# Kernel tuning notes

Hardware: AMD Instinct MI355X
Metric: run time of the kernel (lower is better)

The kernel has to match this reference:

```python
import jax, jax.numpy as jnp
import numpy as np

B, H, NQ, NL, NA = 262144, 256, 4, 2, 16


def _apply_1q(s, U, q):
    # s: [B, 2,2,2,2]; U: [B,2,2] (batched) or [2,2] (shared)
    s = jnp.moveaxis(s, 1 + q, -1)
    if U.ndim == 3:
        s = jnp.einsum('bij,b...j->b...i', U, s)
    else:
        s = jnp.einsum('ij,b...j->b...i', U, s)
    return jnp.moveaxis(s, -1, 1 + q)


def _apply_cnot(s, c, t):
    s = jnp.moveaxis(s, (1 + c, 1 + t), (-2, -1))
    s = jnp.stack([s[..., 0, :], s[..., 1, ::-1]], axis=-2)  # flip target when control=1
    return jnp.moveaxis(s, (-2, -1), (1 + c, 1 + t))


def _rx(theta):
    # batched RX: theta [B] -> [B,2,2]
    c = jnp.cos(theta / 2).astype(jnp.complex64)
    s = (-1j) * jnp.sin(theta / 2)
    return jnp.stack([jnp.stack([c, s], -1), jnp.stack([s, c], -1)], -2)


def _rot(phi, theta, omega):
    # PennyLane Rot = RZ(omega) @ RY(theta) @ RZ(phi), scalar angles -> [2,2]
    c, s = jnp.cos(theta / 2), jnp.sin(theta / 2)
    return jnp.array(1, jnp.complex64) * jnp.stack([
        jnp.stack([jnp.exp(-0.5j * (phi + omega)) * c, -jnp.exp(0.5j * (phi - omega)) * s], -1),
        jnp.stack([jnp.exp(-0.5j * (phi - omega)) * s, jnp.exp(0.5j * (phi + omega)) * c], -1),
    ], -2)


def _circuit(angles, q_weights):
    # angles: [B, NQ] -> PauliZ expvals [B, NQ] via 4-qubit state-vector sim
    b = angles.shape[0]
    s = jnp.zeros((b,) + (2,) * NQ, jnp.complex64)
    s = s.at[(slice(None),) + (0,) * NQ].set(1.0)
    for q in range(NQ):  # AngleEmbedding (RX rotations)
        s = _apply_1q(s, _rx(angles[:, q]), q)
    for l in range(NL):  # StronglyEntanglingLayers
        for w in range(NQ):
            s = _apply_1q(s, _rot(q_weights[l, w, 0], q_weights[l, w, 1], q_weights[l, w, 2]), w)
        r = l % (NQ - 1) + 1
        for w in range(NQ):
            s = _apply_cnot(s, w, (w + r) % NQ)
    probs = s.real ** 2 + s.imag ** 2  # [B,2,2,2,2]
    zs = []
    axes = tuple(range(1, NQ + 1))
    for q in range(NQ):
        p = probs.sum(tuple(a for a in axes if a != 1 + q))  # [B,2]
        zs.append(p[:, 0] - p[:, 1])
    return jnp.stack(zs, axis=1)


def setup_inputs() -> dict:
    key = jax.random.key(0)
    ks = jax.random.split(key, 6)
    return {
        'h': jax.random.normal(ks[0], (B, H), jnp.float32),
        'W_embed': jax.random.normal(ks[1], (NQ, H), jnp.float32) / np.sqrt(H),
        'b_embed': jnp.zeros((NQ,), jnp.float32),
        'q_weights': jax.random.uniform(ks[2], (NL, NQ, 3), jnp.float32, 0.0, 2 * np.pi),
        'W_out': jax.random.normal(ks[3], (NA, NQ), jnp.float32) / np.sqrt(NQ),
        'b_out': jnp.zeros((NA,), jnp.float32),
    }


def reference(h, W_embed, b_embed, q_weights, W_out, b_out):
    angles = jnp.tanh(h @ W_embed.T + b_embed)  # [B, NQ]
    z = _circuit(angles, q_weights)             # [B, NQ]
    return z @ W_out.T + b_out                  # [B, NA]
```

## Files before the change

### kernel.cpp

```cpp
#include <hip/hip_runtime.h>

#define NQ 4
#define NL 2
#define NA 16
#define HDIM 256
#define BLK 64
#define RPB 64

template<int PATTERN>
__device__ __forceinline__ float swz_add(float x) {
    return x + __int_as_float(__builtin_amdgcn_ds_swizzle(__float_as_int(x), PATTERN));
}

template<int M>
__device__ __forceinline__ void apply_u(float* sr, float* si, const float* u) {
    const float u00r = u[0], u00i = u[1], u01r = u[2], u01i = u[3];
    const float u10r = u[4], u10i = u[5], u11r = u[6], u11i = u[7];
#pragma unroll
    for (int k = 0; k < 16; ++k) {
        if (k & M) continue;
        const int k1 = k | M;
        const float a0r = sr[k],  a0i = si[k];
        const float a1r = sr[k1], a1i = si[k1];
        sr[k]  = u00r*a0r - u00i*a0i + u01r*a1r - u01i*a1i;
        si[k]  = u00r*a0i + u00i*a0r + u01r*a1i + u01i*a1r;
        sr[k1] = u10r*a0r - u10i*a0i + u11r*a1r - u11i*a1i;
        si[k1] = u10r*a0i + u10i*a0r + u11r*a1i + u11i*a1r;
    }
}

template<int MC, int MT>
__device__ __forceinline__ void cnot(float* sr, float* si) {
#pragma unroll
    for (int k = 0; k < 16; ++k) {
        if ((k & MC) && !(k & MT)) {
            const int k1 = k | MT;
            float tr = sr[k]; sr[k] = sr[k1]; sr[k1] = tr;
            float ti = si[k]; si[k] = si[k1]; si[k1] = ti;
        }
    }
}

__global__ __launch_bounds__(BLK) void qph_kernel(
    const float* __restrict__ h,
    const float* __restrict__ W_embed,
    const float* __restrict__ b_embed,
    const float* __restrict__ q_weights,
    const float* __restrict__ W_out,
    const float* __restrict__ b_out,
    float* __restrict__ out,
    int B)
{
    __shared__ __align__(16) float w_lds[NQ * HDIM];
    __shared__ float rot_lds[NL * NQ][8];
    __shared__ float wout_lds[NA * NQ];
    __shared__ float bout_lds[NA];

    const int tid = threadIdx.x;
    const long rowBase = (long)blockIdx.x * RPB;

#pragma unroll
    for (int k = 0; k < 16; ++k) w_lds[tid + k * BLK] = W_embed[tid + k * BLK];
    if (tid < NA * NQ) wout_lds[tid] = W_out[tid];
    if (tid < NA)      bout_lds[tid] = b_out[tid];
    if (tid < NL * NQ) {
        const float phi = q_weights[tid * 3 + 0];
        const float th  = q_weights[tid * 3 + 1];
        const float om  = q_weights[tid * 3 + 2];
        const float c  = cosf(0.5f * th), s  = sinf(0.5f * th);
        const float al = 0.5f * (phi + om), be = 0.5f * (phi - om);
        const float ca = cosf(al), sa = sinf(al);
        const float cb = cosf(be), sb = sinf(be);
        rot_lds[tid][0] =  ca * c;  rot_lds[tid][1] = -sa * c;
        rot_lds[tid][2] = -cb * s;  rot_lds[tid][3] = -sb * s;
        rot_lds[tid][4] =  cb * s;  rot_lds[tid][5] = -sb * s;
        rot_lds[tid][6] =  ca * c;  rot_lds[tid][7] =  sa * c;
    }
    __syncthreads();

    const int t = tid & 3;
    const int g = tid >> 2;
    const float be0 = b_embed[0], be1 = b_embed[1], be2 = b_embed[2], be3 = b_embed[3];

    long r0 = rowBase + g * 4 + 0; if (r0 >= B) r0 = B - 1;
    long r1 = rowBase + g * 4 + 1; if (r1 >= B) r1 = B - 1;
    long r2 = rowBase + g * 4 + 2; if (r2 >= B) r2 = B - 1;
    long r3 = rowBase + g * 4 + 3; if (r3 >= B) r3 = B - 1;
    const float4* __restrict__ h4 = (const float4*)h;
    const long b0 = r0 * 64, b1 = r1 * 64, b2 = r2 * 64, b3 = r3 * 64;

    float acc[4][4];
#pragma unroll
    for (int rr = 0; rr < 4; ++rr)
#pragma unroll
        for (int q = 0; q < 4; ++q) acc[rr][q] = 0.f;

#pragma unroll
    for (int j = 0; j < 16; ++j) {
        const int col = j * 16 + t * 4;
        const float4 w0 = *(const float4*)&w_lds[0 * HDIM + col];
        const float4 w1 = *(const float4*)&w_lds[1 * HDIM + col];
        const float4 w2 = *(const float4*)&w_lds[2 * HDIM + col];
        const float4 w3 = *(const float4*)&w_lds[3 * HDIM + col];
        const float4 h0 = h4[b0 + j * 4 + t];
        const float4 h1 = h4[b1 + j * 4 + t];
        const float4 h2 = h4[b2 + j * 4 + t];
        const float4 h3 = h4[b3 + j * 4 + t];
#define ACCUM(RR, HV) \
        acc[RR][0] = fmaf(HV.x, w0.x, fmaf(HV.y, w0.y, fmaf(HV.z, w0.z, fmaf(HV.w, w0.w, acc[RR][0])))); \
        acc[RR][1] = fmaf(HV.x, w1.x, fmaf(HV.y, w1.y, fmaf(HV.z, w1.z, fmaf(HV.w, w1.w, acc[RR][1])))); \
        acc[RR][2] = fmaf(HV.x, w2.x, fmaf(HV.y, w2.y, fmaf(HV.z, w2.z, fmaf(HV.w, w2.w, acc[RR][2])))); \
        acc[RR][3] = fmaf(HV.x, w3.x, fmaf(HV.y, w3.y, fmaf(HV.z, w3.z, fmaf(HV.w, w3.w, acc[RR][3]))))
        ACCUM(0, h0);
        ACCUM(1, h1);
        ACCUM(2, h2);
        ACCUM(3, h3);
#undef ACCUM
    }

    float my0 = 0.f, my1 = 0.f, my2 = 0.f, my3 = 0.f;
#pragma unroll
    for (int rr = 0; rr < 4; ++rr) {
        float v0 = acc[rr][0], v1 = acc[rr][1], v2 = acc[rr][2], v3 = acc[rr][3];
        v0 = swz_add<0x041F>(v0); v0 = swz_add<0x081F>(v0);
        v1 = swz_add<0x041F>(v1); v1 = swz_add<0x081F>(v1);
        v2 = swz_add<0x041F>(v2); v2 = swz_add<0x081F>(v2);
        v3 = swz_add<0x041F>(v3); v3 = swz_add<0x081F>(v3);
        if (t == rr) { my0 = v0; my1 = v1; my2 = v2; my3 = v3; }
    }

    const long grow = rowBase + tid;
    if (grow >= B) return;

    const float angs[4] = {tanhf(my0 + be0), tanhf(my1 + be1),
                           tanhf(my2 + be2), tanhf(my3 + be3)};

    float sr[16], si[16];
#pragma unroll
    for (int k = 0; k < 16; ++k) { sr[k] = 0.f; si[k] = 0.f; }
    sr[0] = 1.0f;

#pragma unroll
    for (int q = 0; q < NQ; ++q) {
        const float th = angs[q];
        const float c = __cosf(0.5f * th), s = __sinf(0.5f * th);
        const int m = 8 >> q;
#pragma unroll
        for (int k = 0; k < 16; ++k) {
            if (k & m) continue;
            const int k1 = k | m;
            const float a0r = sr[k],  a0i = si[k];
            const float a1r = sr[k1], a1i = si[k1];
            sr[k]  = c * a0r + s * a1i;
            si[k]  = c * a0i - s * a1r;
            sr[k1] = s * a0i + c * a1r;
            si[k1] = c * a1i - s * a0r;
        }
    }

    apply_u<8>(sr, si, rot_lds[0]);
    apply_u<4>(sr, si, rot_lds[1]);
    apply_u<2>(sr, si, rot_lds[2]);
    apply_u<1>(sr, si, rot_lds[3]);
    cnot<8, 4>(sr, si);
    cnot<4, 2>(sr, si);
    cnot<2, 1>(sr, si);
    cnot<1, 8>(sr, si);
    apply_u<8>(sr, si, rot_lds[4]);
    apply_u<4>(sr, si, rot_lds[5]);
    apply_u<2>(sr, si, rot_lds[6]);
    apply_u<1>(sr, si, rot_lds[7]);
    cnot<8, 2>(sr, si);
    cnot<4, 1>(sr, si);
    cnot<2, 8>(sr, si);
    cnot<1, 4>(sr, si);

    float p[16];
#pragma unroll
    for (int k = 0; k < 16; ++k) p[k] = sr[k] * sr[k] + si[k] * si[k];
    float z[4];
#pragma unroll
    for (int q = 0; q < NQ; ++q) {
        const int m = 8 >> q;
        float zz = 0.f;
#pragma unroll
        for (int k = 0; k < 16; ++k) zz += (k & m) ? -p[k] : p[k];
        z[q] = zz;
    }

    float4* out4 = (float4*)(out + grow * (long)NA);
#pragma unroll
    for (int i = 0; i < 4; ++i) {
        float o[4];
#pragma unroll
        for (int jj = 0; jj < 4; ++jj) {
            const int a = i * 4 + jj;
            float v = bout_lds[a];
#pragma unroll
            for (int q = 0; q < NQ; ++q) v = fmaf(z[q], wout_lds[a * 4 + q], v);
            o[jj] = v;
        }
        out4[i] = make_float4(o[0], o[1], o[2], o[3]);
    }
}

extern "C" void kernel_launch(void* const* d_in, const int* in_sizes, int n_in,
                              void* d_out, int out_size, void* d_ws, size_t ws_size,
                              hipStream_t stream) {
    const float* h         = (const float*)d_in[0];
    const float* W_embed   = (const float*)d_in[1];
    const float* b_embed   = (const float*)d_in[2];
    const float* q_weights = (const float*)d_in[3];
    const float* W_out     = (const float*)d_in[4];
    const float* b_out     = (const float*)d_in[5];
    float* out = (float*)d_out;

    const int B = in_sizes[0] / HDIM;
    const int blocks = (B + RPB - 1) / RPB;
    qph_kernel<<<blocks, BLK, 0, stream>>>(h, W_embed, b_embed, q_weights, W_out, b_out, out, B);
}
```

Measured before the change: 54.25 us.

## Split fused kernel into separate angle-projection and circuit-simulation kernels

Splits the single fused kernel into two launches. The first computes the embedding matmul and tanh, then writes the per-row angles to workspace. The second runs the 4-qubit state-vector simulation and output projection with 256-thread blocks. The aim is to decouple the memory-bound h streaming from the register-heavy simulation, so each kernel can reach better occupancy. The cost is an extra launch and a global round trip of the angles (16 bytes per row).

```diff
diff --git a/kernel.cpp b/kernel.cpp
--- a/kernel.cpp
+++ b/kernel.cpp
@@ -4,78 +4,29 @@
 #define NL 2
 #define NA 16
 #define HDIM 256
-#define BLK 64
-#define RPB 64
+#define BLKA 64
+#define RPBA 64
+#define BLKB 256
 
 template<int PATTERN>
 __device__ __forceinline__ float swz_add(float x) {
     return x + __int_as_float(__builtin_amdgcn_ds_swizzle(__float_as_int(x), PATTERN));
 }
 
-template<int M>
-__device__ __forceinline__ void apply_u(float* sr, float* si, const float* u) {
-    const float u00r = u[0], u00i = u[1], u01r = u[2], u01i = u[3];
-    const float u10r = u[4], u10i = u[5], u11r = u[6], u11i = u[7];
-#pragma unroll
-    for (int k = 0; k < 16; ++k) {
-        if (k & M) continue;
-        const int k1 = k | M;
-        const float a0r = sr[k],  a0i = si[k];
-        const float a1r = sr[k1], a1i = si[k1];
-        sr[k]  = u00r*a0r - u00i*a0i + u01r*a1r - u01i*a1i;
-        si[k]  = u00r*a0i + u00i*a0r + u01r*a1i + u01i*a1r;
-        sr[k1] = u10r*a0r - u10i*a0i + u11r*a1r - u11i*a1i;
-        si[k1] = u10r*a0i + u10i*a0r + u11r*a1i + u11i*a1r;
-    }
-}
-
-template<int MC, int MT>
-__device__ __forceinline__ void cnot(float* sr, float* si) {
-#pragma unroll
-    for (int k = 0; k < 16; ++k) {
-        if ((k & MC) && !(k & MT)) {
-            const int k1 = k | MT;
-            float tr = sr[k]; sr[k] = sr[k1]; sr[k1] = tr;
-            float ti = si[k]; si[k] = si[k1]; si[k1] = ti;
-        }
-    }
-}
-
-__global__ __launch_bounds__(BLK) void qph_kernel(
+__global__ __launch_bounds__(BLKA, 8) void qph_angles(
     const float* __restrict__ h,
     const float* __restrict__ W_embed,
     const float* __restrict__ b_embed,
-    const float* __restrict__ q_weights,
-    const float* __restrict__ W_out,
-    const float* __restrict__ b_out,
-    float* __restrict__ out,
+    float* __restrict__ angs,
     int B)
 {
     __shared__ __align__(16) float w_lds[NQ * HDIM];
-    __shared__ float rot_lds[NL * NQ][8];
-    __shared__ float wout_lds[NA * NQ];
-    __shared__ float bout_lds[NA];
 
     const int tid = threadIdx.x;
-    const long rowBase = (long)blockIdx.x * RPB;
-
-#pragma unroll
-    for (int k = 0; k < 16; ++k) w_lds[tid + k * BLK] = W_embed[tid + k * BLK];
-    if (tid < NA * NQ) wout_lds[tid] = W_out[tid];
-    if (tid < NA)      bout_lds[tid] = b_out[tid];
-    if (tid < NL * NQ) {
-        const float phi = q_weights[tid * 3 + 0];
-        const float th  = q_weights[tid * 3 + 1];
-        const float om  = q_weights[tid * 3 + 2];
-        const float c  = cosf(0.5f * th), s  = sinf(0.5f * th);
-        const float al = 0.5f * (phi + om), be = 0.5f * (phi - om);
-        const float ca = cosf(al), sa = sinf(al);
-        const float cb = cosf(be), sb = sinf(be);
-        rot_lds[tid][0] =  ca * c;  rot_lds[tid][1] = -sa * c;
-        rot_lds[tid][2] = -cb * s;  rot_lds[tid][3] = -sb * s;
-        rot_lds[tid][4] =  cb * s;  rot_lds[tid][5] = -sb * s;
-        rot_lds[tid][6] =  ca * c;  rot_lds[tid][7] =  sa * c;
-    }
+    const long rowBase = (long)blockIdx.x * RPBA;
+
+#pragma unroll
+    for (int k = 0; k < 16; ++k) w_lds[tid + k * BLKA] = W_embed[tid + k * BLKA];
     __syncthreads();
 
     const int t = tid & 3;
@@ -130,10 +81,76 @@
     }
 
     const long grow = rowBase + tid;
+    if (grow < B) {
+        ((float4*)angs)[grow] = make_float4(tanhf(my0 + be0), tanhf(my1 + be1),
+                                            tanhf(my2 + be2), tanhf(my3 + be3));
+    }
+}
+
+template<int M>
+__device__ __forceinline__ void apply_u(float* sr, float* si, const float* u) {
+    const float u00r = u[0], u00i = u[1], u01r = u[2], u01i = u[3];
+    const float u10r = u[4], u10i = u[5], u11r = u[6], u11i = u[7];
+#pragma unroll
+    for (int k = 0; k < 16; ++k) {
+        if (k & M) continue;
+        const int k1 = k | M;
+        const float a0r = sr[k],  a0i = si[k];
+        const float a1r = sr[k1], a1i = si[k1];
+        sr[k]  = u00r*a0r - u00i*a0i + u01r*a1r - u01i*a1i;
+        si[k]  = u00r*a0i + u00i*a0r + u01r*a1i + u01i*a1r;
+        sr[k1] = u10r*a0r - u10i*a0i + u11r*a1r - u11i*a1i;
+        si[k1] = u10r*a0i + u10i*a0r + u11r*a1i + u11i*a1r;
+    }
+}
+
+template<int MC, int MT>
+__device__ __forceinline__ void cnot(float* sr, float* si) {
+#pragma unroll
+    for (int k = 0; k < 16; ++k) {
+        if ((k & MC) && !(k & MT)) {
+            const int k1 = k | MT;
+            float tr = sr[k]; sr[k] = sr[k1]; sr[k1] = tr;
+            float ti = si[k]; si[k] = si[k1]; si[k1] = ti;
+        }
+    }
+}
+
+__global__ __launch_bounds__(BLKB) void qph_sim(
+    const float* __restrict__ angs,
+    const float* __restrict__ q_weights,
+    const float* __restrict__ W_out,
+    const float* __restrict__ b_out,
+    float* __restrict__ out,
+    int B)
+{
+    __shared__ float rot_lds[NL * NQ][8];
+    __shared__ float wout_lds[NA * NQ];
+    __shared__ float bout_lds[NA];
+
+    const int tid = threadIdx.x;
+    if (tid < NA * NQ) wout_lds[tid] = W_out[tid];
+    if (tid < NA)      bout_lds[tid] = b_out[tid];
+    if (tid < NL * NQ) {
+        const float phi = q_weights[tid * 3 + 0];
+        const float th  = q_weights[tid * 3 + 1];
+        const float om  = q_weights[tid * 3 + 2];
+        const float c  = cosf(0.5f * th), s  = sinf(0.5f * th);
+        const float al = 0.5f * (phi + om), be = 0.5f * (phi - om);
+        const float ca = cosf(al), sa = sinf(al);
+        const float cb = cosf(be), sb = sinf(be);
+        rot_lds[tid][0] =  ca * c;  rot_lds[tid][1] = -sa * c;
+        rot_lds[tid][2] = -cb * s;  rot_lds[tid][3] = -sb * s;
+        rot_lds[tid][4] =  cb * s;  rot_lds[tid][5] = -sb * s;
+        rot_lds[tid][6] =  ca * c;  rot_lds[tid][7] =  sa * c;
+    }
+    __syncthreads();
+
+    const long grow = (long)blockIdx.x * BLKB + tid;
     if (grow >= B) return;
 
-    const float angs[4] = {tanhf(my0 + be0), tanhf(my1 + be1),
-                           tanhf(my2 + be2), tanhf(my3 + be3)};
+    const float4 av = ((const float4*)angs)[grow];
+    const float angs_r[4] = {av.x, av.y, av.z, av.w};
 
     float sr[16], si[16];
 #pragma unroll
@@ -142,7 +159,7 @@
 
 #pragma unroll
     for (int q = 0; q < NQ; ++q) {
-        const float th = angs[q];
+        const float th = angs_r[q];
         const float c = __cosf(0.5f * th), s = __sinf(0.5f * th);
         const int m = 8 >> q;
 #pragma unroll
@@ -213,9 +230,12 @@
     const float* q_weights = (const float*)d_in[3];
     const float* W_out     = (const float*)d_in[4];
     const float* b_out     = (const float*)d_in[5];
-    float* out = (float*)d_out;
+    float* out  = (float*)d_out;
+    float* angs = (float*)d_ws;
 
     const int B = in_sizes[0] / HDIM;
-    const int blocks = (B + RPB - 1) / RPB;
-    qph_kernel<<<blocks, BLK, 0, stream>>>(h, W_embed, b_embed, q_weights, W_out, b_out, out, B);
-}
+    const int blocksA = (B + RPBA - 1) / RPBA;
+    const int blocksB = (B + BLKB - 1) / BLKB;
+    qph_angles<<<blocksA, BLKA, 0, stream>>>(h, W_embed, b_embed, angs, B);
+    qph_sim<<<blocksB, BLKB, 0, stream>>>(angs, q_weights, W_out, b_out, out, B);
+}
```

New measurement: 84.04 us. 1.55x slower.
